# Kernel optimization log

Hardware: AMD Instinct MI355X
Metric: run time of the kernel (lower is better)

## Reference

```python
import jax, jax.numpy as jnp
import numpy as np

N_NODES = 50000
N_EDGES = 1600000
IN_CH = 32
HID = 64
EPS = 1e-12


def setup_inputs() -> dict:
    key = jax.random.key(0)
    ks = jax.random.split(key, 10)
    x = jax.random.normal(ks[0], (N_NODES, IN_CH), dtype=jnp.float32)
    edge_index = jax.random.randint(ks[1], (2, N_EDGES), 0, N_NODES, dtype=jnp.int64)

    def lin(k, fan_in, fan_out):
        bound = 1.0 / np.sqrt(fan_in)
        return jax.random.uniform(k, (fan_in, fan_out), jnp.float32, -bound, bound)

    params = {
        # SAGEConv layer 0: lin_l (aggregated neighbors, with bias), lin_r (root, no bias)
        'Wl0': lin(ks[2], IN_CH, HID), 'b0': jnp.zeros((HID,), jnp.float32),
        'Wr0': lin(ks[3], IN_CH, HID),
        # SAGEConv layer 1
        'Wl1': lin(ks[4], HID, HID), 'b1': jnp.zeros((HID,), jnp.float32),
        'Wr1': lin(ks[5], HID, HID),
        # classifier: Linear(64,32) -> ReLU -> Linear(32,1)
        'Wc1': lin(ks[6], HID, HID // 2), 'bc1': jnp.zeros((HID // 2,), jnp.float32),
        'Wc2': lin(ks[7], HID // 2, 1), 'bc2': jnp.zeros((1,), jnp.float32),
    }
    return {'x': x, 'edge_index': edge_index, **params}


def _sage_conv(x, src, dst, Wl, Wr, b):
    # gather messages from source nodes, mean-aggregate at destination
    msg = x[src]                                            # [E, C]
    agg = jax.ops.segment_sum(msg, dst, num_segments=N_NODES)
    cnt = jax.ops.segment_sum(jnp.ones((src.shape[0], 1), x.dtype), dst,
                              num_segments=N_NODES)
    mean = agg / jnp.maximum(cnt, 1.0)                      # [N, C]
    out = mean @ Wl + x @ Wr + b                            # [N, H]
    # normalize=True -> L2 row-normalization (F.normalize, eps=1e-12)
    nrm = jnp.linalg.norm(out, axis=-1, keepdims=True)
    return out / jnp.maximum(nrm, EPS)


def reference(x, edge_index, Wl0, b0, Wr0, Wl1, b1, Wr1, Wc1, bc1, Wc2, bc2):
    src, dst = edge_index[0], edge_index[1]
    h = _sage_conv(x, src, dst, Wl0, Wr0, b0)
    h = jax.nn.relu(h)                                      # dropout inactive (eval)
    h = _sage_conv(h, src, dst, Wl1, Wr1, b1)
    h = jax.nn.relu(h @ Wc1 + bc1)
    logits = (h @ Wc2 + bc2).squeeze(-1)                    # [N]
    return logits
```

## Files before the change

### kernel.cpp

```cpp
#include <hip/hip_runtime.h>

static constexpr int N_NODES = 50000;
static constexpr int N_EDGES = 1600000;
static constexpr int CIN = 32;
static constexpr int HID = 64;
static constexpr int NBUCK = (N_NODES + 31) / 32;
static constexpr int NB_BLD = 128;
static constexpr int EPB2 = N_EDGES / NB_BLD;
static constexpr int NTB2 = (N_NODES + 63) / 64;

__device__ __forceinline__ unsigned short f2bf(float f) {
    unsigned int u = __float_as_uint(f);
    u = (u + 0x7fffu + ((u >> 16) & 1u)) >> 16;
    return (unsigned short)u;
}
__device__ __forceinline__ float bfhi(unsigned int u) { return __uint_as_float(u & 0xffff0000u); }
__device__ __forceinline__ float bflo(unsigned int u) { return __uint_as_float(u << 16); }


__global__ void __launch_bounds__(256)
histB_kernel(const int* __restrict__ ei, int* __restrict__ part) {
    __shared__ int hist[NBUCK];
    for (int i = threadIdx.x; i < NBUCK; i += 256) hist[i] = 0;
    __syncthreads();
    const int base = blockIdx.x * EPB2;
    const int t = threadIdx.x;
    for (int i0 = 0; i0 < EPB2; i0 += 1024) {
        int d[4];
#pragma unroll
        for (int k = 0; k < 4; ++k) {
            const int i = i0 + k * 256 + t;
            d[k] = (i < EPB2) ? ei[N_EDGES + base + i] : -1;
        }
#pragma unroll
        for (int k = 0; k < 4; ++k)
            if (d[k] >= 0) atomicAdd(&hist[d[k] >> 5], 1);
    }
    __syncthreads();
    for (int i = threadIdx.x; i < NBUCK; i += 256)
        part[i * NB_BLD + blockIdx.x] = hist[i];
}

__global__ void __launch_bounds__(NB_BLD)
scanA_kernel(int* __restrict__ part, int* __restrict__ btot) {
    __shared__ int s[NB_BLD];
    const int t = threadIdx.x;
    const int v = part[blockIdx.x * NB_BLD + t];
    s[t] = v;
    __syncthreads();
    for (int st = 1; st < NB_BLD; st <<= 1) {
        int u = (t >= st) ? s[t - st] : 0;
        __syncthreads();
        s[t] += u;
        __syncthreads();
    }
    part[blockIdx.x * NB_BLD + t] = s[t] - v;
    if (t == NB_BLD - 1) btot[blockIdx.x] = s[NB_BLD - 1];
}

__global__ void __launch_bounds__(1024)
scanB_kernel(const int* __restrict__ btot, int* __restrict__ bstart) {
    __shared__ int pairs[1024];
    __shared__ int v0s[1024];
    const int t = threadIdx.x;
    const int i0 = 2 * t, i1 = 2 * t + 1;
    const int v0 = (i0 < NBUCK) ? btot[i0] : 0;
    const int v1 = (i1 < NBUCK) ? btot[i1] : 0;
    v0s[t] = v0;
    const int p = v0 + v1;
    pairs[t] = p;
    __syncthreads();
    for (int st = 1; st < 1024; st <<= 1) {
        int u = (t >= st) ? pairs[t - st] : 0;
        __syncthreads();
        pairs[t] += u;
        __syncthreads();
    }
    const int base = pairs[t] - p;
    if (i0 < NBUCK) bstart[i0] = base;
    if (i1 < NBUCK) bstart[i1] = base + v0s[t];
    if (t == 1023) bstart[NBUCK] = pairs[1023];
}

__global__ void __launch_bounds__(256)
scatterB_kernel(const int* __restrict__ ei, const int* __restrict__ part,
                const int* __restrict__ bstart, unsigned* __restrict__ bentry) {
    __shared__ int cur[NBUCK];
    for (int i = threadIdx.x; i < NBUCK; i += 256)
        cur[i] = bstart[i] + part[i * NB_BLD + blockIdx.x];
    __syncthreads();
    const int base = blockIdx.x * EPB2;
    const int t = threadIdx.x;
    for (int i0 = 0; i0 < EPB2; i0 += 1024) {
        int s[4], d[4];
#pragma unroll
        for (int k = 0; k < 4; ++k) {
            const int i = i0 + k * 256 + t;
            const bool val = i < EPB2;
            s[k] = val ? ei[base + i] : 0;
            d[k] = val ? ei[N_EDGES + base + i] : -1;
        }
#pragma unroll
        for (int k = 0; k < 4; ++k)
            if (d[k] >= 0) {
                const int pos = atomicAdd(&cur[d[k] >> 5], 1);
                bentry[pos] = ((unsigned)s[k] << 5) | (unsigned)(d[k] & 31);
            }
    }
}

__global__ void __launch_bounds__(256)
sortW_kernel(const unsigned* __restrict__ bentry, const int* __restrict__ bstart,
             int* __restrict__ sorted_src, int* __restrict__ off) {
    __shared__ int cnt[32];
    __shared__ int base[33];
    __shared__ int cur[32];
    const int b = blockIdx.x, t = threadIdx.x;
    const int s0 = bstart[b], s1 = bstart[b + 1];
    if (t < 32) cnt[t] = 0;
    __syncthreads();
    for (int i = s0 + t; i < s1; i += 256)
        atomicAdd(&cnt[bentry[i] & 31], 1);
    __syncthreads();
    if (t == 0) {
        int run = s0;
#pragma unroll
        for (int l = 0; l < 32; ++l) { base[l] = run; cur[l] = run; run += cnt[l]; }
        base[32] = run;
    }
    __syncthreads();
    if (t <= 32) {
        const int gn = b * 32 + t;
        if (gn <= N_NODES) off[gn] = base[t];
    }
    for (int i = s0 + t; i < s1; i += 256) {
        const unsigned e = bentry[i];
        const int pos = atomicAdd(&cur[e & 31], 1);
        sorted_src[pos] = (int)(e >> 5);
    }
}

__global__ void __launch_bounds__(256)
agg0_kernel(const float* __restrict__ x,
            const int* __restrict__ off, const int* __restrict__ src,
            unsigned short* __restrict__ mean0b) {
    const int node = blockIdx.x * 4 + (threadIdx.x >> 6);
    const int lane = threadIdx.x & 63;
    if (node >= N_NODES) return;
    const int e0 = off[node], e1 = off[node + 1];
    const int deg = e1 - e0;
    const int grp = lane >> 3, cg = lane & 7;

    float a[4] = {0, 0, 0, 0};
    for (int base = e0; base < e1; base += 64) {
        const int cnt = min(64, e1 - base);
        const int p = base + lane;
        const int sidx = (p < e1) ? src[p] : 0;
        const int nb = (cnt + 7) >> 3;
        float4 u[8];
#pragma unroll
        for (int t = 0; t < 8; ++t) u[t] = make_float4(0.f, 0.f, 0.f, 0.f);
#pragma unroll
        for (int t = 0; t < 8; ++t) {
            if (t < nb) {
                const int pos = (t << 3) | grp;
                const int s = __shfl(sidx, pos);
                if (pos < cnt)
                    u[t] = *reinterpret_cast<const float4*>(x + (size_t)s * CIN + cg * 4);
            }
        }
#pragma unroll
        for (int t = 0; t < 8; ++t) {
            a[0] += u[t].x; a[1] += u[t].y; a[2] += u[t].z; a[3] += u[t].w;
        }
    }
#pragma unroll
    for (int j = 0; j < 4; ++j) {
        a[j] += __shfl_xor(a[j], 8);
        a[j] += __shfl_xor(a[j], 16);
        a[j] += __shfl_xor(a[j], 32);
    }
    const float inv = 1.0f / fmaxf((float)deg, 1.0f);
    if (grp == 0) {
        uint2 o;
        o.x = (unsigned)f2bf(a[0] * inv) | ((unsigned)f2bf(a[1] * inv) << 16);
        o.y = (unsigned)f2bf(a[2] * inv) | ((unsigned)f2bf(a[3] * inv) << 16);
        reinterpret_cast<uint2*>(mean0b)[node * 8 + cg] = o;
    }
}

__global__ void __launch_bounds__(256)
agg1_kernel(const unsigned short* __restrict__ hb,
            const int* __restrict__ off, const int* __restrict__ src,
            float* __restrict__ mean1f) {
    const int node = blockIdx.x * 4 + (threadIdx.x >> 6);
    const int lane = threadIdx.x & 63;
    if (node >= N_NODES) return;
    const int e0 = off[node], e1 = off[node + 1];
    const int deg = e1 - e0;
    const int grp = lane >> 3, cg = lane & 7;

    float a[8] = {0, 0, 0, 0, 0, 0, 0, 0};
    for (int base = e0; base < e1; base += 64) {
        const int cnt = min(64, e1 - base);
        const int p = base + lane;
        const int sidx = (p < e1) ? src[p] : 0;
        const int nb = (cnt + 7) >> 3;
        uint4 u[8];
#pragma unroll
        for (int t = 0; t < 8; ++t) u[t] = make_uint4(0u, 0u, 0u, 0u);
#pragma unroll
        for (int t = 0; t < 8; ++t) {
            if (t < nb) {
                const int pos = (t << 3) | grp;
                const int s = __shfl(sidx, pos);
                if (pos < cnt)
                    u[t] = *reinterpret_cast<const uint4*>(hb + (size_t)s * HID + cg * 8);
            }
        }
#pragma unroll
        for (int t = 0; t < 8; ++t) {
            a[0] += bflo(u[t].x); a[1] += bfhi(u[t].x);
            a[2] += bflo(u[t].y); a[3] += bfhi(u[t].y);
            a[4] += bflo(u[t].z); a[5] += bfhi(u[t].z);
            a[6] += bflo(u[t].w); a[7] += bfhi(u[t].w);
        }
    }
#pragma unroll
    for (int j = 0; j < 8; ++j) {
        a[j] += __shfl_xor(a[j], 8);
        a[j] += __shfl_xor(a[j], 16);
        a[j] += __shfl_xor(a[j], 32);
    }
    const float inv = 1.0f / fmaxf((float)deg, 1.0f);
    if (grp == 0) {
        float4 o1 = make_float4(a[0] * inv, a[1] * inv, a[2] * inv, a[3] * inv);
        float4 o2 = make_float4(a[4] * inv, a[5] * inv, a[6] * inv, a[7] * inv);
        float4* dst = reinterpret_cast<float4*>(mean1f + (size_t)node * HID + cg * 8);
        dst[0] = o1; dst[1] = o2;
    }
}

__global__ void __launch_bounds__(256)
transform0_kernel(const float* __restrict__ x,
                  const unsigned short* __restrict__ mean0b,
                  const float* __restrict__ Wl0, const float* __restrict__ Wr0,
                  const float* __restrict__ b0,
                  unsigned short* __restrict__ hb) {
    __shared__ float sWl[CIN * HID];
    __shared__ float sWr[CIN * HID];
    const int t = threadIdx.x;
    reinterpret_cast<float4*>(sWl)[t]       = reinterpret_cast<const float4*>(Wl0)[t];
    reinterpret_cast<float4*>(sWl)[t + 256] = reinterpret_cast<const float4*>(Wl0)[t + 256];
    reinterpret_cast<float4*>(sWr)[t]       = reinterpret_cast<const float4*>(Wr0)[t];
    reinterpret_cast<float4*>(sWr)[t + 256] = reinterpret_cast<const float4*>(Wr0)[t + 256];
    __syncthreads();

    const int lane = t & 63, wid = t >> 6;
    const int cg = lane & 15, rep = lane >> 4;
    const int nbase = blockIdx.x * 64 + wid * 16 + rep;
    const float4 bv = reinterpret_cast<const float4*>(b0)[cg];
    float acc[4][4];
#pragma unroll
    for (int s = 0; s < 4; ++s) {
        acc[s][0] = bv.x; acc[s][1] = bv.y; acc[s][2] = bv.z; acc[s][3] = bv.w;
    }
    for (int kc = 0; kc < CIN; kc += 4) {
        float4 wl4[4], wr4[4];
#pragma unroll
        for (int kk = 0; kk < 4; ++kk) {
            wl4[kk] = *reinterpret_cast<const float4*>(sWl + (kc + kk) * HID + 4 * cg);
            wr4[kk] = *reinterpret_cast<const float4*>(sWr + (kc + kk) * HID + 4 * cg);
        }
#pragma unroll
        for (int s = 0; s < 4; ++s) {
            const int n = nbase + 4 * s;
            if (n < N_NODES) {
                const uint2 mu = *reinterpret_cast<const uint2*>(mean0b + (size_t)n * CIN + kc);
                const float4 xv = *reinterpret_cast<const float4*>(x + (size_t)n * CIN + kc);
                const float m4[4] = {bflo(mu.x), bfhi(mu.x), bflo(mu.y), bfhi(mu.y)};
                const float x4[4] = {xv.x, xv.y, xv.z, xv.w};
#pragma unroll
                for (int kk = 0; kk < 4; ++kk) {
                    acc[s][0] = fmaf(m4[kk], wl4[kk].x, fmaf(x4[kk], wr4[kk].x, acc[s][0]));
                    acc[s][1] = fmaf(m4[kk], wl4[kk].y, fmaf(x4[kk], wr4[kk].y, acc[s][1]));
                    acc[s][2] = fmaf(m4[kk], wl4[kk].z, fmaf(x4[kk], wr4[kk].z, acc[s][2]));
                    acc[s][3] = fmaf(m4[kk], wl4[kk].w, fmaf(x4[kk], wr4[kk].w, acc[s][3]));
                }
            }
        }
    }
#pragma unroll
    for (int s = 0; s < 4; ++s) {
        float ss = acc[s][0] * acc[s][0] + acc[s][1] * acc[s][1] +
                   acc[s][2] * acc[s][2] + acc[s][3] * acc[s][3];
        ss += __shfl_xor(ss, 1);
        ss += __shfl_xor(ss, 2);
        ss += __shfl_xor(ss, 4);
        ss += __shfl_xor(ss, 8);
        const float sc = 1.0f / fmaxf(sqrtf(ss), 1e-12f);
        const int n = nbase + 4 * s;
        if (n < N_NODES) {
            uint2 o;
            o.x = (unsigned)f2bf(fmaxf(acc[s][0] * sc, 0.f)) |
                  ((unsigned)f2bf(fmaxf(acc[s][1] * sc, 0.f)) << 16);
            o.y = (unsigned)f2bf(fmaxf(acc[s][2] * sc, 0.f)) |
                  ((unsigned)f2bf(fmaxf(acc[s][3] * sc, 0.f)) << 16);
            *reinterpret_cast<uint2*>(hb + (size_t)n * HID + cg * 4) = o;
        }
    }
}

static constexpr int SVP = 68;
__global__ void __launch_bounds__(256)
transform1_kernel(const unsigned short* __restrict__ hb,
                  const float* __restrict__ mean1f,
                  const float* __restrict__ Wl1, const float* __restrict__ Wr1,
                  const float* __restrict__ b1,
                  const float* __restrict__ Wc1, const float* __restrict__ bc1,
                  const float* __restrict__ Wc2, const float* __restrict__ bc2,
                  float* __restrict__ out) {
    __shared__ float sWl[HID * HID];
    __shared__ float sWr[HID * HID];
    __shared__ float sWc[HID * 32];
    __shared__ float sV[64 * SVP];
    const int t = threadIdx.x;
#pragma unroll
    for (int i = 0; i < 4; ++i) {
        reinterpret_cast<float4*>(sWl)[t + 256 * i] = reinterpret_cast<const float4*>(Wl1)[t + 256 * i];
        reinterpret_cast<float4*>(sWr)[t + 256 * i] = reinterpret_cast<const float4*>(Wr1)[t + 256 * i];
    }
#pragma unroll
    for (int i = 0; i < 2; ++i)
        reinterpret_cast<float4*>(sWc)[t + 256 * i] = reinterpret_cast<const float4*>(Wc1)[t + 256 * i];
    __syncthreads();

    const int lane = t & 63, wid = t >> 6;
    const int cg = lane & 15, rep = lane >> 4;
    const int nbase = blockIdx.x * 64 + wid * 16 + rep;
    const float4 bv = reinterpret_cast<const float4*>(b1)[cg];
    float acc[4][4];
#pragma unroll
    for (int s = 0; s < 4; ++s) {
        acc[s][0] = bv.x; acc[s][1] = bv.y; acc[s][2] = bv.z; acc[s][3] = bv.w;
    }
    for (int kc = 0; kc < HID; kc += 4) {
        float4 wl4[4], wr4[4];
#pragma unroll
        for (int kk = 0; kk < 4; ++kk) {
            wl4[kk] = *reinterpret_cast<const float4*>(sWl + (kc + kk) * HID + 4 * cg);
            wr4[kk] = *reinterpret_cast<const float4*>(sWr + (kc + kk) * HID + 4 * cg);
        }
#pragma unroll
        for (int s = 0; s < 4; ++s) {
            const int n = nbase + 4 * s;
            if (n < N_NODES) {
                const float4 mv = *reinterpret_cast<const float4*>(mean1f + (size_t)n * HID + kc);
                const uint2 hu = *reinterpret_cast<const uint2*>(hb + (size_t)n * HID + kc);
                const float m4[4] = {mv.x, mv.y, mv.z, mv.w};
                const float h4[4] = {bflo(hu.x), bfhi(hu.x), bflo(hu.y), bfhi(hu.y)};
#pragma unroll
                for (int kk = 0; kk < 4; ++kk) {
                    acc[s][0] = fmaf(m4[kk], wl4[kk].x, fmaf(h4[kk], wr4[kk].x, acc[s][0]));
                    acc[s][1] = fmaf(m4[kk], wl4[kk].y, fmaf(h4[kk], wr4[kk].y, acc[s][1]));
                    acc[s][2] = fmaf(m4[kk], wl4[kk].z, fmaf(h4[kk], wr4[kk].z, acc[s][2]));
                    acc[s][3] = fmaf(m4[kk], wl4[kk].w, fmaf(h4[kk], wr4[kk].w, acc[s][3]));
                }
            }
        }
    }
#pragma unroll
    for (int s = 0; s < 4; ++s) {
        float ss = acc[s][0] * acc[s][0] + acc[s][1] * acc[s][1] +
                   acc[s][2] * acc[s][2] + acc[s][3] * acc[s][3];
        ss += __shfl_xor(ss, 1);
        ss += __shfl_xor(ss, 2);
        ss += __shfl_xor(ss, 4);
        ss += __shfl_xor(ss, 8);
        const float sc = 1.0f / fmaxf(sqrtf(ss), 1e-12f);
        const int ln = wid * 16 + rep + 4 * s;
        sV[ln * SVP + 4 * cg + 0] = acc[s][0] * sc;
        sV[ln * SVP + 4 * cg + 1] = acc[s][1] * sc;
        sV[ln * SVP + 4 * cg + 2] = acc[s][2] * sc;
        sV[ln * SVP + 4 * cg + 3] = acc[s][3] * sc;
    }
    __syncthreads();

    const int n2 = t >> 2, ig = t & 3;
    float c1[8];
#pragma unroll
    for (int u = 0; u < 8; ++u) c1[u] = bc1[ig * 8 + u];
#pragma unroll 4
    for (int c = 0; c < HID; ++c) {
        const float vv = sV[n2 * SVP + c];
        const float4 w0 = *reinterpret_cast<const float4*>(sWc + c * 32 + ig * 8);
        const float4 w1 = *reinterpret_cast<const float4*>(sWc + c * 32 + ig * 8 + 4);
        c1[0] = fmaf(vv, w0.x, c1[0]);
        c1[1] = fmaf(vv, w0.y, c1[1]);
        c1[2] = fmaf(vv, w0.z, c1[2]);
        c1[3] = fmaf(vv, w0.w, c1[3]);
        c1[4] = fmaf(vv, w1.x, c1[4]);
        c1[5] = fmaf(vv, w1.y, c1[5]);
        c1[6] = fmaf(vv, w1.z, c1[6]);
        c1[7] = fmaf(vv, w1.w, c1[7]);
    }
    float pp = 0.f;
#pragma unroll
    for (int u = 0; u < 8; ++u)
        pp = fmaf(fmaxf(c1[u], 0.f), Wc2[ig * 8 + u], pp);
    pp += __shfl_xor(pp, 1);
    pp += __shfl_xor(pp, 2);
    const int g = blockIdx.x * 64 + n2;
    if (ig == 0 && g < N_NODES) out[g] = pp + bc2[0];
}

extern "C" void kernel_launch(void* const* d_in, const int* in_sizes, int n_in,
                              void* d_out, int out_size, void* d_ws, size_t ws_size,
                              hipStream_t stream) {
    const float* x   = (const float*)d_in[0];
    const int*   ei  = (const int*)d_in[1];
    const float* Wl0 = (const float*)d_in[2];
    const float* b0  = (const float*)d_in[3];
    const float* Wr0 = (const float*)d_in[4];
    const float* Wl1 = (const float*)d_in[5];
    const float* b1  = (const float*)d_in[6];
    const float* Wr1 = (const float*)d_in[7];
    const float* Wc1 = (const float*)d_in[8];
    const float* bc1 = (const float*)d_in[9];
    const float* Wc2 = (const float*)d_in[10];
    const float* bc2 = (const float*)d_in[11];
    float* out = (float*)d_out;

    float* W = (float*)d_ws;
    int*            part   = (int*)W;
    int*            btot   = (int*)(W + 200064);
    int*            bstart = (int*)(W + 201632);
    unsigned*       bentry = (unsigned*)(W + 1600000);
    unsigned short* mean0b = (unsigned short*)W;
    float*          mean1f = W;
    int*            sorted_src = (int*)(W + 3200000);
    int*            off    = (int*)(W + 4800000);
    unsigned short* hb     = (unsigned short*)(W + 4850016);

    const int T = 256;
    histB_kernel<<<NB_BLD, T, 0, stream>>>(ei, part);
    scanA_kernel<<<NBUCK, NB_BLD, 0, stream>>>(part, btot);
    scanB_kernel<<<1, 1024, 0, stream>>>(btot, bstart);
    scatterB_kernel<<<NB_BLD, T, 0, stream>>>(ei, part, bstart, bentry);
    sortW_kernel<<<NBUCK, T, 0, stream>>>(bentry, bstart, sorted_src, off);

    const int ngrid = (N_NODES + 3) / 4;
    agg0_kernel<<<ngrid, T, 0, stream>>>(x, off, sorted_src, mean0b);
    transform0_kernel<<<NTB2, T, 0, stream>>>(x, mean0b, Wl0, Wr0, b0, hb);
    agg1_kernel<<<ngrid, T, 0, stream>>>(hb, off, sorted_src, mean1f);
    transform1_kernel<<<NTB2, T, 0, stream>>>(hb, mean1f, Wl1, Wr1, b1,
                                              Wc1, bc1, Wc2, bc2, out);
}
```

Before: 164.1 us.

## Fuse bucket sort with layer-0 aggregation using shared-memory source list

Merges the per-bucket counting sort into the first mean-aggregation kernel. Each block keeps its sorted source indices as 16-bit values in shared memory and reads them from there, instead of a separate kernel re-reading sorted_src and offsets from global memory. The aim is to save one launch and a round trip through global memory. In exchange each wave aggregates 8 nodes one after another, so the aggregation grid is far smaller and latency hiding is reduced. Buckets with more than SMAX edges would read shared memory out of bounds. Separately, transform1 drops its shared-memory copy of Wc1 and reads it straight from global memory.

```diff
diff --git a/kernel.cpp b/kernel.cpp
--- a/kernel.cpp
+++ b/kernel.cpp
@@ -8,6 +8,7 @@
 static constexpr int NB_BLD = 128;
 static constexpr int EPB2 = N_EDGES / NB_BLD;
 static constexpr int NTB2 = (N_NODES + 63) / 64;
+static constexpr int SMAX = 3072;
 
 __device__ __forceinline__ unsigned short f2bf(float f) {
     unsigned int u = __float_as_uint(f);
@@ -110,20 +111,24 @@
 }
 
 __global__ void __launch_bounds__(256)
-sortW_kernel(const unsigned* __restrict__ bentry, const int* __restrict__ bstart,
-             int* __restrict__ sorted_src, int* __restrict__ off) {
+agg0s_kernel(const float* __restrict__ x,
+             const unsigned* __restrict__ bentry, const int* __restrict__ bstart,
+             int* __restrict__ sorted_src, int* __restrict__ off,
+             unsigned short* __restrict__ mean0b) {
     __shared__ int cnt[32];
     __shared__ int base[33];
     __shared__ int cur[32];
+    __shared__ unsigned short sSrc[SMAX];
     const int b = blockIdx.x, t = threadIdx.x;
     const int s0 = bstart[b], s1 = bstart[b + 1];
+    const int m = s1 - s0;
     if (t < 32) cnt[t] = 0;
     __syncthreads();
-    for (int i = s0 + t; i < s1; i += 256)
-        atomicAdd(&cnt[bentry[i] & 31], 1);
+    for (int i = t; i < m; i += 256)
+        atomicAdd(&cnt[bentry[s0 + i] & 31], 1);
     __syncthreads();
     if (t == 0) {
-        int run = s0;
+        int run = 0;
 #pragma unroll
         for (int l = 0; l < 32; ++l) { base[l] = run; cur[l] = run; run += cnt[l]; }
         base[32] = run;
@@ -131,61 +136,60 @@
     __syncthreads();
     if (t <= 32) {
         const int gn = b * 32 + t;
-        if (gn <= N_NODES) off[gn] = base[t];
-    }
-    for (int i = s0 + t; i < s1; i += 256) {
-        const unsigned e = bentry[i];
+        if (gn <= N_NODES) off[gn] = s0 + base[t];
+    }
+    for (int i = t; i < m; i += 256) {
+        const unsigned e = bentry[s0 + i];
         const int pos = atomicAdd(&cur[e & 31], 1);
-        sorted_src[pos] = (int)(e >> 5);
-    }
-}
-
-__global__ void __launch_bounds__(256)
-agg0_kernel(const float* __restrict__ x,
-            const int* __restrict__ off, const int* __restrict__ src,
-            unsigned short* __restrict__ mean0b) {
-    const int node = blockIdx.x * 4 + (threadIdx.x >> 6);
-    const int lane = threadIdx.x & 63;
-    if (node >= N_NODES) return;
-    const int e0 = off[node], e1 = off[node + 1];
-    const int deg = e1 - e0;
+        const int srcv = (int)(e >> 5);
+        if (pos < SMAX) sSrc[pos] = (unsigned short)srcv;
+        sorted_src[s0 + pos] = srcv;
+    }
+    __syncthreads();
+
+    const int lane = t & 63, wid = t >> 6;
     const int grp = lane >> 3, cg = lane & 7;
-
-    float a[4] = {0, 0, 0, 0};
-    for (int base = e0; base < e1; base += 64) {
-        const int cnt = min(64, e1 - base);
-        const int p = base + lane;
-        const int sidx = (p < e1) ? src[p] : 0;
-        const int nb = (cnt + 7) >> 3;
-        float4 u[8];
-#pragma unroll
-        for (int t = 0; t < 8; ++t) u[t] = make_float4(0.f, 0.f, 0.f, 0.f);
-#pragma unroll
-        for (int t = 0; t < 8; ++t) {
-            if (t < nb) {
-                const int pos = (t << 3) | grp;
-                const int s = __shfl(sidx, pos);
-                if (pos < cnt)
-                    u[t] = *reinterpret_cast<const float4*>(x + (size_t)s * CIN + cg * 4);
-            }
-        }
-#pragma unroll
-        for (int t = 0; t < 8; ++t) {
-            a[0] += u[t].x; a[1] += u[t].y; a[2] += u[t].z; a[3] += u[t].w;
-        }
-    }
-#pragma unroll
-    for (int j = 0; j < 4; ++j) {
-        a[j] += __shfl_xor(a[j], 8);
-        a[j] += __shfl_xor(a[j], 16);
-        a[j] += __shfl_xor(a[j], 32);
-    }
-    const float inv = 1.0f / fmaxf((float)deg, 1.0f);
-    if (grp == 0) {
-        uint2 o;
-        o.x = (unsigned)f2bf(a[0] * inv) | ((unsigned)f2bf(a[1] * inv) << 16);
-        o.y = (unsigned)f2bf(a[2] * inv) | ((unsigned)f2bf(a[3] * inv) << 16);
-        reinterpret_cast<uint2*>(mean0b)[node * 8 + cg] = o;
+#pragma unroll
+    for (int j = 0; j < 8; ++j) {
+        const int l = wid * 8 + j;
+        const int e0 = base[l], e1 = base[l + 1];
+        const int deg = e1 - e0;
+        float a[4] = {0, 0, 0, 0};
+        for (int be = e0; be < e1; be += 64) {
+            const int cnt_ = min(64, e1 - be);
+            const int nb = (cnt_ + 7) >> 3;
+            float4 u[8];
+#pragma unroll
+            for (int tt = 0; tt < 8; ++tt) u[tt] = make_float4(0.f, 0.f, 0.f, 0.f);
+#pragma unroll
+            for (int tt = 0; tt < 8; ++tt) {
+                if (tt < nb) {
+                    const int pos = be + ((tt << 3) | grp);
+                    if (pos < e1) {
+                        const int s = (int)sSrc[pos];
+                        u[tt] = *reinterpret_cast<const float4*>(x + (size_t)s * CIN + cg * 4);
+                    }
+                }
+            }
+#pragma unroll
+            for (int tt = 0; tt < 8; ++tt) {
+                a[0] += u[tt].x; a[1] += u[tt].y; a[2] += u[tt].z; a[3] += u[tt].w;
+            }
+        }
+#pragma unroll
+        for (int jj = 0; jj < 4; ++jj) {
+            a[jj] += __shfl_xor(a[jj], 8);
+            a[jj] += __shfl_xor(a[jj], 16);
+            a[jj] += __shfl_xor(a[jj], 32);
+        }
+        const float inv = 1.0f / fmaxf((float)deg, 1.0f);
+        const int gn = b * 32 + l;
+        if (grp == 0 && gn < N_NODES) {
+            uint2 o;
+            o.x = (unsigned)f2bf(a[0] * inv) | ((unsigned)f2bf(a[1] * inv) << 16);
+            o.y = (unsigned)f2bf(a[2] * inv) | ((unsigned)f2bf(a[3] * inv) << 16);
+            reinterpret_cast<uint2*>(mean0b)[gn * 8 + cg] = o;
+        }
     }
 }
 
@@ -322,7 +326,6 @@
                   float* __restrict__ out) {
     __shared__ float sWl[HID * HID];
     __shared__ float sWr[HID * HID];
-    __shared__ float sWc[HID * 32];
     __shared__ float sV[64 * SVP];
     const int t = threadIdx.x;
 #pragma unroll
@@ -330,9 +333,6 @@
         reinterpret_cast<float4*>(sWl)[t + 256 * i] = reinterpret_cast<const float4*>(Wl1)[t + 256 * i];
         reinterpret_cast<float4*>(sWr)[t + 256 * i] = reinterpret_cast<const float4*>(Wr1)[t + 256 * i];
     }
-#pragma unroll
-    for (int i = 0; i < 2; ++i)
-        reinterpret_cast<float4*>(sWc)[t + 256 * i] = reinterpret_cast<const float4*>(Wc1)[t + 256 * i];
     __syncthreads();
 
     const int lane = t & 63, wid = t >> 6;
@@ -393,8 +393,8 @@
 #pragma unroll 4
     for (int c = 0; c < HID; ++c) {
         const float vv = sV[n2 * SVP + c];
-        const float4 w0 = *reinterpret_cast<const float4*>(sWc + c * 32 + ig * 8);
-        const float4 w1 = *reinterpret_cast<const float4*>(sWc + c * 32 + ig * 8 + 4);
+        const float4 w0 = *reinterpret_cast<const float4*>(Wc1 + c * 32 + ig * 8);
+        const float4 w1 = *reinterpret_cast<const float4*>(Wc1 + c * 32 + ig * 8 + 4);
         c1[0] = fmaf(vv, w0.x, c1[0]);
         c1[1] = fmaf(vv, w0.y, c1[1]);
         c1[2] = fmaf(vv, w0.z, c1[2]);
@@ -447,11 +447,10 @@
     scanA_kernel<<<NBUCK, NB_BLD, 0, stream>>>(part, btot);
     scanB_kernel<<<1, 1024, 0, stream>>>(btot, bstart);
     scatterB_kernel<<<NB_BLD, T, 0, stream>>>(ei, part, bstart, bentry);
-    sortW_kernel<<<NBUCK, T, 0, stream>>>(bentry, bstart, sorted_src, off);
-
+
+    agg0s_kernel<<<NBUCK, T, 0, stream>>>(x, bentry, bstart, sorted_src, off, mean0b);
+    transform0_kernel<<<NTB2, T, 0, stream>>>(x, mean0b, Wl0, Wr0, b0, hb);
     const int ngrid = (N_NODES + 3) / 4;
-    agg0_kernel<<<ngrid, T, 0, stream>>>(x, off, sorted_src, mean0b);
-    transform0_kernel<<<NTB2, T, 0, stream>>>(x, mean0b, Wl0, Wr0, b0, hb);
     agg1_kernel<<<ngrid, T, 0, stream>>>(hb, off, sorted_src, mean1f);
     transform1_kernel<<<NTB2, T, 0, stream>>>(hb, mean1f, Wl1, Wr1, b1,
                                               Wc1, bc1, Wc2, bc2, out);
```

After: 160.7 us. -2.1%, faster.
